# Optimization experiments

Hardware: AMD Instinct MI355X
Metric: run time of the kernel (lower is better)

Reference implementation:

```python
import jax, jax.numpy as jnp
import numpy as np

TRIM_RATIO = 0.1
B, N, D_IN, D_H, N_OUT, D_OUT = 64, 1024, 512, 1024, 10, 1


def setup_inputs() -> dict:
    key = jax.random.key(0)
    ks = jax.random.split(key, 10)
    X = jax.random.normal(ks[0], (B, N, D_IN), dtype=jnp.float32)
    # ragged valid lengths in [N//2, N]; guarantees num_valid > 2*k for trim_ratio=0.1
    lengths = jax.random.randint(ks[1], (B,), N // 2, N + 1)
    mask = (jnp.arange(N)[None, :] < lengths[:, None]).astype(jnp.float32)
    s_in, s_h = 1.0 / np.sqrt(D_IN), 1.0 / np.sqrt(D_H)
    W1 = jax.random.uniform(ks[2], (D_IN, D_H), jnp.float32, -s_in, s_in)
    b1 = jax.random.uniform(ks[3], (D_H,), jnp.float32, -s_in, s_in)
    W2 = jax.random.uniform(ks[4], (D_H, D_H), jnp.float32, -s_h, s_h)
    b2 = jax.random.uniform(ks[5], (D_H,), jnp.float32, -s_h, s_h)
    W3 = jax.random.uniform(ks[6], (D_H, D_H), jnp.float32, -s_h, s_h)
    b3 = jax.random.uniform(ks[7], (D_H,), jnp.float32, -s_h, s_h)
    W4 = jax.random.uniform(ks[8], (D_H, N_OUT * D_OUT), jnp.float32, -s_h, s_h)
    b4 = jax.random.uniform(ks[9], (N_OUT * D_OUT,), jnp.float32, -s_h, s_h)
    return {"X": X, "mask": mask, "W1": W1, "b1": b1, "W2": W2, "b2": b2,
            "W3": W3, "b3": b3, "W4": W4, "b4": b4}


def reference(X, mask, W1, b1, W2, b2, W3, b3, W4, b4):
    # encode MLP: [B,N,D_IN] -> [B,N,D_H]
    encoded = jax.nn.relu(jnp.einsum('bni,ih->bnh', X, W1) + b1) @ W2 + b2
    masked = encoded * mask[..., None]
    num_valid = mask.sum(axis=-1).astype(jnp.int32)                 # [B]
    k = (num_valid.astype(jnp.float32) * TRIM_RATIO).astype(jnp.int32)  # floor, as int()
    # push invalid rows to +inf so valid elements occupy the first num_valid slots after sort
    padded = jnp.where(mask[..., None] > 0, masked, jnp.inf)
    sorted_v = jnp.sort(padded, axis=1)                             # per-column sort, [B,N,D_H]
    pos = jnp.arange(N)[None, :]
    keep = (pos >= k[:, None]) & (pos < (num_valid - k)[:, None])   # [B,N]
    summed = jnp.sum(jnp.where(keep[..., None], sorted_v, 0.0), axis=1)  # [B,D_H]
    denom = (num_valid - 2 * k).astype(jnp.float32)[:, None]
    aggregated = summed / denom                                     # trimmed mean
    # decode MLP
    out = jax.nn.relu(aggregated @ W3 + b3) @ W4 + b4               # [B, N_OUT*D_OUT]
    out = out.reshape(-1, N_OUT, D_OUT).squeeze(-1)                 # [B, N_OUT]
    return out
```

## Files before the change

### kernel.cpp

```cpp
#include <hip/hip_runtime.h>


typedef _Float16 half8  __attribute__((ext_vector_type(8)));
typedef _Float16 half4v __attribute__((ext_vector_type(4)));
typedef float    floatx4 __attribute__((ext_vector_type(4)));

#define GLD_LDS(g, l)                                                                     \
  __builtin_amdgcn_global_load_lds((const __attribute__((address_space(1))) void*)(g),    \
                                   (__attribute__((address_space(3))) void*)(l), 16, 0, 0)

__global__ void prep_nv(const float* __restrict__ mask, int* __restrict__ nv_arr,
                        int* __restrict__ k_arr) {
  int b = blockIdx.x, lane = threadIdx.x;
  const float4* mp = (const float4*)(mask + (b << 10));
  float s = 0.f;
#pragma unroll
  for (int i = 0; i < 4; ++i) {
    float4 v = mp[lane + i * 64];
    s += v.x + v.y + v.z + v.w;
  }
#pragma unroll
  for (int off = 32; off > 0; off >>= 1) s += __shfl_xor(s, off, 64);
  if (lane == 0) {
    int nv = (int)(s + 0.5f);
    int kk = (int)((float)nv * 0.1f);
    nv_arr[b] = nv;
    k_arr[b] = kk;
  }
}

__device__ __forceinline__ void transpose_body(const float* __restrict__ W,
                                               _Float16* __restrict__ WT, int R, int C,
                                               int r0, int c0, _Float16 (*tile)[65]) {
  for (int i = threadIdx.x; i < 4096; i += 256) {
    int r = i >> 6, c = i & 63;
    tile[r][c] = (_Float16)W[(size_t)(r0 + r) * C + c0 + c];
  }
  __syncthreads();
  for (int i = threadIdx.x; i < 4096; i += 256) {
    int c = i >> 6, r = i & 63;
    WT[(size_t)(c0 + c) * R + r0 + r] = tile[r][c];
  }
}

__global__ __launch_bounds__(256) void preprocess(
    const float* __restrict__ X, _Float16* __restrict__ X16,
    const float* __restrict__ W1, _Float16* __restrict__ W1T,
    const float* __restrict__ W2, _Float16* __restrict__ W2T,
    const int* __restrict__ nv_arr) {
  __shared__ _Float16 tile[64][65];
  int bid = blockIdx.x;
  if (bid < 16384) {
    int n0 = (bid << 2) & 1023;
    int batch = bid >> 8;
    int nv = nv_arr[batch];
    if (n0 >= ((nv + 255) & ~255)) return;
    int i = (bid * 256 + threadIdx.x) * 8;
    float4 a = *(const float4*)(X + i);
    float4 c = *(const float4*)(X + i + 4);
    half8 h;
    h[0] = (_Float16)a.x; h[1] = (_Float16)a.y; h[2] = (_Float16)a.z; h[3] = (_Float16)a.w;
    h[4] = (_Float16)c.x; h[5] = (_Float16)c.y; h[6] = (_Float16)c.z; h[7] = (_Float16)c.w;
    *(half8*)(X16 + i) = h;
  } else if (bid < 16384 + 128) {
    int id = bid - 16384;
    transpose_body(W1, W1T, 512, 1024, (id & 7) * 64, (id >> 3) * 64, tile);
  } else {
    int id = bid - 16512;
    transpose_body(W2, W2T, 1024, 1024, (id & 15) * 64, (id >> 4) * 64, tile);
  }
}

template <int KDIM, int MODE>
__global__ __launch_bounds__(512, 2) void gemm_kernel(
    const _Float16* __restrict__ Aop, const _Float16* __restrict__ Bop,
    const float* __restrict__ bias, const int* __restrict__ nv_arr,
    _Float16* __restrict__ outp) {
  constexpr int NT = KDIM / 64;
  __shared__ __align__(16) _Float16 lds[2][2][256 * 64];

  int bid = blockIdx.x;
  int fat = ((((bid >> 5) << 3) | (bid & 7))) << 8;
  int thin = ((bid >> 3) & 3) << 8;
  int i0, j0;
  if (MODE == 1) {
    i0 = thin; j0 = fat;
    if ((j0 & 1023) >= nv_arr[j0 >> 10]) return;
  } else {
    i0 = fat; j0 = thin;
    if ((i0 & 1023) >= nv_arr[i0 >> 10]) return;
  }
  const int t = threadIdx.x, lane = t & 63;
  const int wv = t >> 6, wm = wv & 1, wn = wv >> 1;
  const int lr = lane & 15, q = lane >> 4;
  const int swz = (q ^ (lr & 7)) * 8;

  const int gch = (t & 7) ^ ((t >> 3) & 7);
  const _Float16* gA = Aop + (size_t)(i0 + (t >> 3)) * KDIM + gch * 8;
  const _Float16* gB = Bop + (size_t)(j0 + (t >> 3)) * KDIM + gch * 8;

#define STG(OP, BUF, KT, R)                                                   \
  GLD_LDS(((OP) ? gB : gA) + (size_t)(R) * 64 * KDIM + (size_t)(KT) * 64,     \
          &lds[BUF][OP][((R) * 512 + (t & ~63)) * 8])

  floatx4 acc[8][4] = {};
  half8 af[4][2];
  half8 bf[2][2][2];

#define LD_A(BUF, IH)                                                         \
  _Pragma("unroll") for (int f = 0; f < 4; ++f)                               \
  _Pragma("unroll") for (int kk = 0; kk < 2; ++kk)                            \
      af[f][kk] = *(const half8*)&lds[BUF][0]                                 \
          [(((wm << 7) + ((IH) << 6) + (f << 4) + lr) << 6) + (swz ^ (kk << 5))];

#define LD_B_HALF(BUF, JH)                                                    \
  _Pragma("unroll") for (int g = 0; g < 2; ++g)                               \
  _Pragma("unroll") for (int kk = 0; kk < 2; ++kk)                            \
      bf[JH][g][kk] = *(const half8*)&lds[BUF][1]                             \
          [(((wn << 6) + ((JH) << 5) + (g << 4) + lr) << 6) + (swz ^ (kk << 5))];

#define MFMA_QUAD(IH, JH)                                                     \
  __builtin_amdgcn_s_setprio(1);                                              \
  _Pragma("unroll") for (int f = 0; f < 4; ++f)                               \
  _Pragma("unroll") for (int g = 0; g < 2; ++g)                               \
  _Pragma("unroll") for (int kk = 0; kk < 2; ++kk)                            \
      acc[((IH) << 2) + f][((JH) << 1) + g] =                                 \
          __builtin_amdgcn_mfma_f32_16x16x32_f16(                             \
              af[f][kk], bf[JH][g][kk], acc[((IH) << 2) + f][((JH) << 1) + g], 0, 0, 0); \
  __builtin_amdgcn_s_setprio(0);

#define TILE(KT, CUR, DO_STG, DO_B1)                                          \
  {                                                                           \
    LD_A(CUR, 0);                                                             \
    LD_B_HALF(CUR, 0);                                                        \
    LD_B_HALF(CUR, 1);                                                        \
    MFMA_QUAD(0, 0);                                                          \
    MFMA_QUAD(0, 1);                                                          \
    LD_A(CUR, 1);                                                             \
    asm volatile("s_waitcnt lgkmcnt(0)" ::: "memory");                        \
    __builtin_amdgcn_sched_barrier(0);                                        \
    __builtin_amdgcn_s_barrier();            \
    __builtin_amdgcn_sched_barrier(0);                                        \
    if (DO_STG) { STG(0, CUR, (KT) + 2, 0); STG(0, CUR, (KT) + 2, 1);         \
                  STG(1, CUR, (KT) + 2, 0); STG(1, CUR, (KT) + 2, 1);         \
                  STG(0, CUR, (KT) + 2, 2); STG(0, CUR, (KT) + 2, 3);         \
                  STG(1, CUR, (KT) + 2, 2); STG(1, CUR, (KT) + 2, 3); }       \
    MFMA_QUAD(1, 0);                                                          \
    MFMA_QUAD(1, 1);                                                          \
    if (DO_B1) {                                                              \
      if (DO_STG) { asm volatile("s_waitcnt vmcnt(8)" ::: "memory"); }        \
      else        { asm volatile("s_waitcnt vmcnt(0)" ::: "memory"); }        \
      __builtin_amdgcn_sched_barrier(0);                                      \
      __builtin_amdgcn_s_barrier();                 \
      __builtin_amdgcn_sched_barrier(0);                                      \
    }                                                                         \
  }

  STG(0, 0, 0, 0); STG(0, 0, 0, 1); STG(0, 0, 0, 2); STG(0, 0, 0, 3);
  STG(1, 0, 0, 0); STG(1, 0, 0, 1); STG(1, 0, 0, 2); STG(1, 0, 0, 3);
  STG(0, 1, 1, 0); STG(0, 1, 1, 1); STG(0, 1, 1, 2); STG(0, 1, 1, 3);
  STG(1, 1, 1, 0); STG(1, 1, 1, 1); STG(1, 1, 1, 2); STG(1, 1, 1, 3);
  asm volatile("s_waitcnt vmcnt(8)" ::: "memory");
  __builtin_amdgcn_s_barrier();
  __builtin_amdgcn_sched_barrier(0);

  for (int kt = 0; kt < NT - 2; kt += 2) {
    TILE(kt, 0, 1, 1);
    TILE(kt + 1, 1, 1, 1);
  }
  TILE(NT - 2, 0, 0, 1);
  TILE(NT - 1, 1, 0, 0);

  if (MODE == 1) {
#pragma unroll
    for (int mi = 0; mi < 8; ++mi) {
      int ih = i0 + (wm << 7) + (mi << 4) + (q << 2);
      floatx4 bb = *(const floatx4*)&bias[ih];
#pragma unroll
      for (int nj = 0; nj < 4; ++nj) {
        int j = j0 + (wn << 6) + (nj << 4) + lr;
        floatx4 v = acc[mi][nj];
        half4v hv;
#pragma unroll
        for (int r = 0; r < 4; ++r) hv[r] = (_Float16)fmaxf(v[r] + bb[r], 0.f);
        *(half4v*)&outp[(size_t)j * 1024 + ih] = hv;
      }
    }
  } else {
#pragma unroll
    for (int nj = 0; nj < 4; ++nj) {
      int j = j0 + (wn << 6) + (nj << 4) + lr;
      float bj = bias[j];
#pragma unroll
      for (int mi = 0; mi < 8; ++mi) {
        int im = i0 + (wm << 7) + (mi << 4) + (q << 2);
        int bb = im >> 10, n = im & 1023;
        floatx4 v = acc[mi][nj];
        half4v hv;
#pragma unroll
        for (int r = 0; r < 4; ++r) hv[r] = (_Float16)(v[r] + bj);
        *(half4v*)&outp[((size_t)bb << 20) + ((size_t)j << 10) + (size_t)n] = hv;
      }
    }
  }
}

#define NB 1024
__global__ __launch_bounds__(256) void trim_kernel(const _Float16* __restrict__ encT,
                                                   const int* __restrict__ nv_arr,
                                                   const int* __restrict__ k_arr,
                                                   float* __restrict__ agg) {
  __shared__ unsigned int cnt[4 * NB];
  int t = threadIdx.x, lane = t & 63, w = t >> 6;
  int blk = blockIdx.x;
  int batch = blk >> 8;
  int h = ((blk & 255) << 2) + w;
  unsigned int* cw = cnt + w * NB;
  uint4* cp = (uint4*)cw;
  {
    uint4 z = {0u, 0u, 0u, 0u};
#pragma unroll
    for (int i = 0; i < 4; ++i) cp[lane * 4 + (i ^ ((lane >> 1) & 3))] = z;
  }

  int nv = nv_arr[batch], kk = k_arr[batch];
  const _Float16* col = encT + ((size_t)batch << 20) + ((size_t)h << 10);
  const uint4* p = (const uint4*)col + lane * 2;
  uint4 u0 = p[0], u1 = p[1];
  unsigned vals[8] = {u0.x, u0.y, u0.z, u0.w, u1.x, u1.y, u1.z, u1.w};
  int nvalid = nv - lane * 16;

  float vv[16];
  int bn[16];
#pragma unroll
  for (int d = 0; d < 8; ++d) {
    unsigned u = vals[d];
#pragma unroll
    for (int sub = 0; sub < 2; ++sub) {
      int idx = d * 2 + sub;
      unsigned short bits = (unsigned short)(sub ? (u >> 16) : (u & 0xffffu));
      _Float16 hvv;
      __builtin_memcpy(&hvv, &bits, 2);
      float v = (float)hvv;
      if (idx < nvalid) {
        v = fminf(fmaxf(v, -8.0f), 7.999f);
        int bin = (int)((v + 8.0f) * 64.0f);
        bin = min(NB - 1, bin);
        vv[idx] = v;
        bn[idx] = bin;
        int Lb = bin >> 4, jc = (bin >> 2) & 3;
        int phys = ((Lb << 2) + (jc ^ ((Lb >> 1) & 3))) * 4 + (bin & 3);
        atomicAdd(&cw[phys], 1u);
      } else {
        vv[idx] = 0.f;
        bn[idx] = -1;
      }
    }
  }

  int c[16];
  {
    uint4 rb[4];
#pragma unroll
    for (int i = 0; i < 4; ++i) rb[i] = cp[lane * 4 + (i ^ ((lane >> 1) & 3))];
#pragma unroll
    for (int i = 0; i < 4; ++i) {
      c[4 * i] = (int)rb[i].x; c[4 * i + 1] = (int)rb[i].y;
      c[4 * i + 2] = (int)rb[i].z; c[4 * i + 3] = (int)rb[i].w;
    }
  }
  int ct = 0;
#pragma unroll
  for (int i = 0; i < 16; ++i) ct += c[i];
  int ci = ct;
#pragma unroll
  for (int off = 1; off < 64; off <<= 1) {
    int cu = __shfl_up(ci, off, 64);
    if (lane >= off) ci += cu;
  }
  int cex = ci - ct;
  int r1 = kk, r2 = nv - kk;
  int p1 = -1, p2 = -1;
  {
    int run = cex;
#pragma unroll
    for (int i = 0; i < 16; ++i) {
      int cc = c[i];
      if (run < r1 && r1 <= run + cc) p1 = ((lane * 16 + i) << 12) | run;
      if (run < r2 && r2 <= run + cc) p2 = ((lane * 16 + i) << 12) | run;
      run += cc;
    }
  }
#pragma unroll
  for (int off = 32; off > 0; off >>= 1) {
    p1 = max(p1, __shfl_xor(p1, off, 64));
    p2 = max(p2, __shfl_xor(p2, off, 64));
  }
  int b1 = p1 >> 12, cex1 = p1 & 4095;
  int b2 = p2 >> 12, cex2 = p2 & 4095;
  float s1 = 0.f, s2 = 0.f, tm = 0.f;
  int c1 = 0, c2 = 0;
#pragma unroll
  for (int i = 0; i < 16; ++i) {
    int b = bn[i];
    float v = vv[i];
    if (b == b1) { s1 += v; c1++; }
    if (b == b2) { s2 += v; c2++; }
    if (b > b1 && b < b2) tm += v;
  }
#pragma unroll
  for (int off = 32; off > 0; off >>= 1) {
    s1 += __shfl_xor(s1, off, 64);
    s2 += __shfl_xor(s2, off, 64);
    tm += __shfl_xor(tm, off, 64);
    c1 += __shfl_xor(c1, off, 64);
    c2 += __shfl_xor(c2, off, 64);
  }
  float mid;
  if (b1 == b2) {
    mid = (float)(r2 - r1) * (s1 / (float)c1);
  } else {
    mid = (float)(cex1 + c1 - r1) * (s1 / (float)c1) + tm +
          (float)(r2 - cex2) * (s2 / (float)c2);
  }
  if (lane == 0) {
    agg[(batch << 10) + h] = mid / (float)(nv - 2 * kk);
  }
}

__global__ __launch_bounds__(256) void decode1(const float* __restrict__ agg,
                                               const float* __restrict__ W3,
                                               const float* __restrict__ b3,
                                               float* __restrict__ A3) {
  __shared__ float al[1024];
  __shared__ float red[256];
  int b = blockIdx.x, hb = blockIdx.y, t = threadIdx.x;
  for (int i = t; i < 1024; i += 256) al[i] = agg[(b << 10) + i];
  __syncthreads();
  int hl = t & 63, ks = t >> 6;
  int h = hb * 64 + hl;
  const float* wp = W3 + (size_t)(ks * 256) * 1024 + h;
  const float* ap = al + ks * 256;
  float acc = 0.f;
#pragma unroll 8
  for (int k = 0; k < 256; ++k) acc = fmaf(ap[k], wp[(size_t)k * 1024], acc);
  red[t] = acc;
  __syncthreads();
  if (t < 64) {
    float s = red[t] + red[t + 64] + red[t + 128] + red[t + 192] + b3[hb * 64 + t];
    A3[(b << 10) + hb * 64 + t] = fmaxf(s, 0.f);
  }
}

__global__ void decode2(const float* __restrict__ A3, const float* __restrict__ W4,
                        const float* __restrict__ b4, float* __restrict__ outp) {
  __shared__ float red[4][10];
  int b = blockIdx.x, t = threadIdx.x, lane = t & 63, w = t >> 6;
  float part[10];
#pragma unroll
  for (int o = 0; o < 10; ++o) part[o] = 0.f;
#pragma unroll
  for (int jj = 0; jj < 4; ++jj) {
    int h2 = jj * 256 + t;
    float a = A3[(b << 10) + h2];
#pragma unroll
    for (int o = 0; o < 10; ++o) part[o] = fmaf(a, W4[h2 * 10 + o], part[o]);
  }
#pragma unroll
  for (int o = 0; o < 10; ++o)
#pragma unroll
    for (int off = 32; off > 0; off >>= 1) part[o] += __shfl_xor(part[o], off, 64);
  if (lane == 0)
#pragma unroll
    for (int o = 0; o < 10; ++o) red[w][o] = part[o];
  __syncthreads();
  if (t < 10) outp[b * 10 + t] = b4[t] + red[0][t] + red[1][t] + red[2][t] + red[3][t];
}

extern "C" void kernel_launch(void* const* d_in, const int* in_sizes, int n_in,
                              void* d_out, int out_size, void* d_ws, size_t ws_size,
                              hipStream_t stream) {
  const float* X = (const float*)d_in[0];
  const float* mask = (const float*)d_in[1];
  const float* W1 = (const float*)d_in[2];
  const float* b1 = (const float*)d_in[3];
  const float* W2 = (const float*)d_in[4];
  const float* b2 = (const float*)d_in[5];
  const float* W3 = (const float*)d_in[6];
  const float* b3 = (const float*)d_in[7];
  const float* W4 = (const float*)d_in[8];
  const float* b4 = (const float*)d_in[9];
  float* outp = (float*)d_out;
  char* ws = (char*)d_ws;

  _Float16* X16 = (_Float16*)(ws);
  _Float16* H1 = (_Float16*)(ws + 67108864ull);
  _Float16* encT = (_Float16*)(ws + 201326592ull);
  _Float16* W1T = (_Float16*)(ws + 335544320ull);
  _Float16* W2T = (_Float16*)(ws + 336592896ull);
  float* agg = (float*)(ws + 338690048ull);
  float* A3 = (float*)(ws + 338952192ull);
  int* nv_arr = (int*)(ws + 339214336ull);
  int* k_arr = (int*)(ws + 339214592ull);

  prep_nv<<<64, 64, 0, stream>>>(mask, nv_arr, k_arr);
  preprocess<<<16768, 256, 0, stream>>>(X, X16, W1, W1T, W2, W2T, nv_arr);
  gemm_kernel<512, 1><<<1024, 512, 0, stream>>>(W1T, X16, b1, nv_arr, H1);
  gemm_kernel<1024, 2><<<1024, 512, 0, stream>>>(H1, W2T, b2, nv_arr, encT);
  trim_kernel<<<16384, 256, 0, stream>>>(encT, nv_arr, k_arr, agg);
  decode1<<<dim3(64, 16), 256, 0, stream>>>(agg, W3, b3, A3);
  decode2<<<64, 256, 0, stream>>>(A3, W4, b4, outp);
}
```

Measured before the change: 532.3 us.

## Use smaller-tile GEMM for first layer and histogram-free binary-search trim

Adds a 128x128-tile GEMM variant with 256 threads for the first encoder layer, so row skipping happens at a finer granularity. The X conversion now skips padded rows at a 128-row boundary instead of 256. The trim kernel drops the LDS atomic histogram and finds the two cutoff bins by a wave-wide binary search over bin indices using ballot-style counts. This removes LDS atomic traffic at the cost of more shuffle reductions. The smaller GEMM tile gives up some data reuse and does not double-buffer its loads.

```diff
diff --git a/kernel.cpp b/kernel.cpp
--- a/kernel.cpp
+++ b/kernel.cpp
@@ -54,7 +54,7 @@
     int n0 = (bid << 2) & 1023;
     int batch = bid >> 8;
     int nv = nv_arr[batch];
-    if (n0 >= ((nv + 255) & ~255)) return;
+    if (n0 >= ((nv + 127) & ~127)) return;
     int i = (bid * 256 + threadIdx.x) * 8;
     float4 a = *(const float4*)(X + i);
     float4 c = *(const float4*)(X + i + 4);
@@ -68,6 +68,115 @@
   } else {
     int id = bid - 16512;
     transpose_body(W2, W2T, 1024, 1024, (id & 15) * 64, (id >> 4) * 64, tile);
+  }
+}
+
+template <int KDIM, int MODE>
+__global__ __launch_bounds__(256, 3) void gemm_kernel_sm(
+    const _Float16* __restrict__ Aop, const _Float16* __restrict__ Bop,
+    const float* __restrict__ bias, const int* __restrict__ nv_arr,
+    _Float16* __restrict__ outp) {
+  __shared__ __align__(16) _Float16 ldsA[128 * 64];
+  __shared__ __align__(16) _Float16 ldsB[128 * 64];
+  int i0, j0;
+  int bid = blockIdx.x;
+  int fat = (((bid >> 6) << 3) | (bid & 7)) * 128;
+  int thin = ((bid >> 3) & 7) * 128;
+  if (MODE == 1) {
+    i0 = thin; j0 = fat;
+    if ((j0 & 1023) >= nv_arr[j0 >> 10]) return;
+  } else {
+    i0 = fat; j0 = thin;
+    if ((i0 & 1023) >= nv_arr[i0 >> 10]) return;
+  }
+  const int t = threadIdx.x, lane = t & 63;
+  const int wv = t >> 6, wi = wv & 1, wj = wv >> 1;
+  const int lr = lane & 15, q = lane >> 4;
+
+  floatx4 acc[4][4] = {};
+
+  const int gch = (t & 7) ^ ((t >> 3) & 7);
+  const _Float16* gA[4];
+  const _Float16* gB[4];
+  _Float16* lA[4];
+  _Float16* lB[4];
+#pragma unroll
+  for (int r = 0; r < 4; ++r) {
+    int row = r * 32 + (t >> 3);
+    gA[r] = Aop + (size_t)(i0 + row) * KDIM + gch * 8;
+    gB[r] = Bop + (size_t)(j0 + row) * KDIM + gch * 8;
+    lA[r] = ldsA + (r * 256 + (t & ~63)) * 8;
+    lB[r] = ldsB + (r * 256 + (t & ~63)) * 8;
+  }
+
+  int aoff[4], boff[4];
+#pragma unroll
+  for (int mi = 0; mi < 4; ++mi) {
+    int row = wi * 64 + mi * 16 + lr;
+    aoff[mi] = row * 64 + ((q ^ (row & 7)) * 8);
+  }
+#pragma unroll
+  for (int nj = 0; nj < 4; ++nj) {
+    int row = wj * 64 + nj * 16 + lr;
+    boff[nj] = row * 64 + ((q ^ (row & 7)) * 8);
+  }
+
+  for (int kt = 0; kt < KDIM / 64; ++kt) {
+#pragma unroll
+    for (int r = 0; r < 4; ++r) GLD_LDS(gA[r], lA[r]);
+#pragma unroll
+    for (int r = 0; r < 4; ++r) GLD_LDS(gB[r], lB[r]);
+#pragma unroll
+    for (int r = 0; r < 4; ++r) { gA[r] += 64; gB[r] += 64; }
+    __syncthreads();
+#pragma unroll
+    for (int kk = 0; kk < 2; ++kk) {
+      half8 af[4], bf[4];
+#pragma unroll
+      for (int mi = 0; mi < 4; ++mi) af[mi] = *(const half8*)&ldsA[aoff[mi] ^ (kk * 32)];
+#pragma unroll
+      for (int nj = 0; nj < 4; ++nj) bf[nj] = *(const half8*)&ldsB[boff[nj] ^ (kk * 32)];
+#pragma unroll
+      for (int mi = 0; mi < 4; ++mi)
+#pragma unroll
+        for (int nj = 0; nj < 4; ++nj)
+          acc[mi][nj] =
+              __builtin_amdgcn_mfma_f32_16x16x32_f16(af[mi], bf[nj], acc[mi][nj], 0, 0, 0);
+    }
+    __syncthreads();
+  }
+
+  if (MODE == 1) {
+#pragma unroll
+    for (int mi = 0; mi < 4; ++mi) {
+      int ih = i0 + wi * 64 + mi * 16 + q * 4;
+      floatx4 bb = *(const floatx4*)&bias[ih];
+#pragma unroll
+      for (int nj = 0; nj < 4; ++nj) {
+        int j = j0 + wj * 64 + nj * 16 + lr;
+        floatx4 v = acc[mi][nj];
+        half4v hv;
+#pragma unroll
+        for (int r = 0; r < 4; ++r) hv[r] = (_Float16)fmaxf(v[r] + bb[r], 0.f);
+        *(half4v*)&outp[(size_t)j * 1024 + ih] = hv;
+      }
+    }
+  } else {
+#pragma unroll
+    for (int nj = 0; nj < 4; ++nj) {
+      int j = j0 + wj * 64 + nj * 16 + lr;
+      float bj = bias[j];
+#pragma unroll
+      for (int mi = 0; mi < 4; ++mi) {
+        int im = i0 + wi * 64 + mi * 16 + q * 4;
+        int bb = im >> 10, n = im & 1023;
+        floatx4 v = acc[mi][nj];
+        half4v hv;
+#pragma unroll
+        for (int r = 0; r < 4; ++r) hv[r] = (_Float16)(v[r] + bj);
+        *(half4v*)&outp[((size_t)bb << 20) + ((size_t)j << 10) + (size_t)n] = hv;
+      }
+    }
   }
 }
 
@@ -210,47 +319,35 @@
                                                    const int* __restrict__ nv_arr,
                                                    const int* __restrict__ k_arr,
                                                    float* __restrict__ agg) {
-  __shared__ unsigned int cnt[4 * NB];
   int t = threadIdx.x, lane = t & 63, w = t >> 6;
   int blk = blockIdx.x;
   int batch = blk >> 8;
   int h = ((blk & 255) << 2) + w;
-  unsigned int* cw = cnt + w * NB;
-  uint4* cp = (uint4*)cw;
-  {
-    uint4 z = {0u, 0u, 0u, 0u};
-#pragma unroll
-    for (int i = 0; i < 4; ++i) cp[lane * 4 + (i ^ ((lane >> 1) & 3))] = z;
-  }
-
   int nv = nv_arr[batch], kk = k_arr[batch];
   const _Float16* col = encT + ((size_t)batch << 20) + ((size_t)h << 10);
-  const uint4* p = (const uint4*)col + lane * 2;
-  uint4 u0 = p[0], u1 = p[1];
+  const uint4* p = (const uint4*)col;
+  uint4 u0 = p[lane];
+  uint4 u1 = p[lane + 64];
   unsigned vals[8] = {u0.x, u0.y, u0.z, u0.w, u1.x, u1.y, u1.z, u1.w};
-  int nvalid = nv - lane * 16;
 
   float vv[16];
   int bn[16];
 #pragma unroll
   for (int d = 0; d < 8; ++d) {
     unsigned u = vals[d];
+    int pbase = (d < 4) ? (8 * lane + 2 * d) : (512 + 8 * lane + 2 * (d - 4));
 #pragma unroll
     for (int sub = 0; sub < 2; ++sub) {
-      int idx = d * 2 + sub;
+      int idx = 2 * d + sub;
       unsigned short bits = (unsigned short)(sub ? (u >> 16) : (u & 0xffffu));
       _Float16 hvv;
       __builtin_memcpy(&hvv, &bits, 2);
       float v = (float)hvv;
-      if (idx < nvalid) {
+      if (pbase + sub < nv) {
         v = fminf(fmaxf(v, -8.0f), 7.999f);
-        int bin = (int)((v + 8.0f) * 64.0f);
-        bin = min(NB - 1, bin);
+        int bin = min(NB - 1, (int)((v + 8.0f) * 64.0f));
         vv[idx] = v;
         bn[idx] = bin;
-        int Lb = bin >> 4, jc = (bin >> 2) & 3;
-        int phys = ((Lb << 2) + (jc ^ ((Lb >> 1) & 3))) * 4 + (bin & 3);
-        atomicAdd(&cw[phys], 1u);
       } else {
         vv[idx] = 0.f;
         bn[idx] = -1;
@@ -258,46 +355,44 @@
     }
   }
 
-  int c[16];
+  int r1 = kk, r2 = nv - kk;
+  int b1 = 0, b2 = 0;
+#pragma unroll
+  for (int s = 512; s > 0; s >>= 1) {
+    int cand = b1 + s - 1;
+    int c = 0;
+#pragma unroll
+    for (int i = 0; i < 16; ++i) c += ((unsigned)bn[i] <= (unsigned)cand) ? 1 : 0;
+#pragma unroll
+    for (int off = 32; off > 0; off >>= 1) c += __shfl_xor(c, off, 64);
+    if (c < r1) b1 += s;
+  }
+#pragma unroll
+  for (int s = 512; s > 0; s >>= 1) {
+    int cand = b2 + s - 1;
+    int c = 0;
+#pragma unroll
+    for (int i = 0; i < 16; ++i) c += ((unsigned)bn[i] <= (unsigned)cand) ? 1 : 0;
+#pragma unroll
+    for (int off = 32; off > 0; off >>= 1) c += __shfl_xor(c, off, 64);
+    if (c < r2) b2 += s;
+  }
+
+  int cex1, cex2;
   {
-    uint4 rb[4];
-#pragma unroll
-    for (int i = 0; i < 4; ++i) rb[i] = cp[lane * 4 + (i ^ ((lane >> 1) & 3))];
-#pragma unroll
-    for (int i = 0; i < 4; ++i) {
-      c[4 * i] = (int)rb[i].x; c[4 * i + 1] = (int)rb[i].y;
-      c[4 * i + 2] = (int)rb[i].z; c[4 * i + 3] = (int)rb[i].w;
-    }
-  }
-  int ct = 0;
-#pragma unroll
-  for (int i = 0; i < 16; ++i) ct += c[i];
-  int ci = ct;
-#pragma unroll
-  for (int off = 1; off < 64; off <<= 1) {
-    int cu = __shfl_up(ci, off, 64);
-    if (lane >= off) ci += cu;
-  }
-  int cex = ci - ct;
-  int r1 = kk, r2 = nv - kk;
-  int p1 = -1, p2 = -1;
-  {
-    int run = cex;
+    int ca = 0, cb = 0;
 #pragma unroll
     for (int i = 0; i < 16; ++i) {
-      int cc = c[i];
-      if (run < r1 && r1 <= run + cc) p1 = ((lane * 16 + i) << 12) | run;
-      if (run < r2 && r2 <= run + cc) p2 = ((lane * 16 + i) << 12) | run;
-      run += cc;
-    }
-  }
-#pragma unroll
-  for (int off = 32; off > 0; off >>= 1) {
-    p1 = max(p1, __shfl_xor(p1, off, 64));
-    p2 = max(p2, __shfl_xor(p2, off, 64));
-  }
-  int b1 = p1 >> 12, cex1 = p1 & 4095;
-  int b2 = p2 >> 12, cex2 = p2 & 4095;
+      ca += ((unsigned)bn[i] < (unsigned)b1) ? 1 : 0;
+      cb += ((unsigned)bn[i] < (unsigned)b2) ? 1 : 0;
+    }
+    int packed = ca | (cb << 16);
+#pragma unroll
+    for (int off = 32; off > 0; off >>= 1) packed += __shfl_xor(packed, off, 64);
+    cex1 = packed & 0xffff;
+    cex2 = packed >> 16;
+  }
+
   float s1 = 0.f, s2 = 0.f, tm = 0.f;
   int c1 = 0, c2 = 0;
 #pragma unroll
@@ -308,14 +403,16 @@
     if (b == b2) { s2 += v; c2++; }
     if (b > b1 && b < b2) tm += v;
   }
+  int cpk = c1 | (c2 << 16);
 #pragma unroll
   for (int off = 32; off > 0; off >>= 1) {
     s1 += __shfl_xor(s1, off, 64);
     s2 += __shfl_xor(s2, off, 64);
     tm += __shfl_xor(tm, off, 64);
-    c1 += __shfl_xor(c1, off, 64);
-    c2 += __shfl_xor(c2, off, 64);
-  }
+    cpk += __shfl_xor(cpk, off, 64);
+  }
+  c1 = cpk & 0xffff;
+  c2 = cpk >> 16;
   float mid;
   if (b1 == b2) {
     mid = (float)(r2 - r1) * (s1 / (float)c1);
@@ -405,7 +502,7 @@
 
   prep_nv<<<64, 64, 0, stream>>>(mask, nv_arr, k_arr);
   preprocess<<<16768, 256, 0, stream>>>(X, X16, W1, W1T, W2, W2T, nv_arr);
-  gemm_kernel<512, 1><<<1024, 512, 0, stream>>>(W1T, X16, b1, nv_arr, H1);
+  gemm_kernel_sm<512, 1><<<4096, 256, 0, stream>>>(W1T, X16, b1, nv_arr, H1);
   gemm_kernel<1024, 2><<<1024, 512, 0, stream>>>(H1, W2T, b2, nv_arr, encT);
   trim_kernel<<<16384, 256, 0, stream>>>(encT, nv_arr, k_arr, agg);
   decode1<<<dim3(64, 16), 256, 0, stream>>>(agg, W3, b3, A3);
```

Measured after the change: 606.8 us. +14.0%, slower.
